# Kernel tuning notes

Measured on AMD Instinct MI355X. Metric: run time of the kernel, lower is better.

## Reference

```python
import jax
import jax.numpy as jnp
from jax import lax
import numpy as np

N_COLORS = 256  # n_possible_colors; classifier emits N_COLORS+1 logits (last = 'new color')
LRELU_SLOPE = 0.01  # torch nn.LeakyReLU default negative_slope


def setup_inputs() -> dict:
    key = jax.random.key(0)
    ks = jax.random.split(key, 8)
    N, E = 8192, 512
    deg = 32
    s1 = 1.0 / np.sqrt(2 * E)
    s2 = 1.0 / np.sqrt(E)
    s3 = 1.0 / np.sqrt(400)
    return {
        "embeddings": jax.random.normal(ks[0], (N, E), jnp.float32),
        "neighbors": jax.random.randint(ks[1], (N, deg), 0, N, jnp.int32),
        "W1": jax.random.normal(ks[2], (2 * E, E), jnp.float32) * s1,
        "b1": jnp.zeros((E,), jnp.float32),
        "W2": jax.random.normal(ks[3], (E, 400), jnp.float32) * s2,
        "b2": jnp.zeros((400,), jnp.float32),
        "W3": jax.random.normal(ks[4], (400, N_COLORS + 1), jnp.float32) * s3,
        "b3": jnp.zeros((N_COLORS + 1,), jnp.float32),
        "baseline": jnp.ones((), jnp.float32),
    }


def _leaky(x):
    return jnp.where(x >= 0, x, LRELU_SLOPE * x)


def reference(embeddings, neighbors, W1, b1, W2, b2, W3, b3, baseline):
    N, E = embeddings.shape
    C = N_COLORS + 1  # 257 output classes
    graph_emb = embeddings.mean(axis=0)  # torch.mean(embeddings, dim=0), constant across steps
    idx = jnp.arange(C)
    colors0 = jnp.full((N,), -1, jnp.int32).at[0].set(0)  # _assign_color(0, vertex_order[0])
    key0 = jax.random.key(42)

    def step(carry, v):
        colors, n_used, logp, key = carry
        key, sk = jax.random.split(key)
        # classifier MLP: cat(node_emb, graph_emb) -> 512 -> 400 -> 257
        x = jnp.concatenate([embeddings[v], graph_emb])  # [2E]
        h = _leaky(x @ W1 + b1)
        h = _leaky(h @ W2 + b2)
        logits = h @ W3 + b3  # [257]
        # _mask_irrelevant_colors: disable unused colors in [n_used, 256)
        irrel = (idx >= n_used) & (idx < N_COLORS)
        # _mask_colors: disable colors of already-colored neighbors (-1 = uncolored -> padded out)
        nb_c = colors[neighbors[v]]  # [deg]
        adj_mask = jnp.zeros((C + 1,), bool).at[jnp.where(nb_c < 0, C, nb_c)].set(True)[:C]
        logits = jnp.where(irrel | adj_mask, -jnp.inf, logits)
        probs = jax.nn.softmax(logits)  # classifier output
        raw = jax.random.categorical(sk, logits)  # np.random.choice(p=probs)
        chosen = jnp.where(raw == N_COLORS, n_used, raw).astype(jnp.int32)
        n_used = jnp.where(raw == N_COLORS, n_used + 1, n_used)
        colors = colors.at[v].set(chosen)
        p = probs[raw]
        logp = logp + jnp.log(p + 1e-8) - jnp.log(jnp.asarray(1e-8, p.dtype))
        return (colors, n_used, logp, key), None

    init = (colors0, jnp.int32(1), jnp.float32(0.0), key0)
    (colors, n_used, logp, _), _ = lax.scan(step, init, jnp.arange(1, N))
    loss = (n_used.astype(jnp.float32) - baseline) * logp / N
    return colors, loss
```

## Files before the change

### kernel.cpp

```cpp
#include <hip/hip_runtime.h>
#include <stdint.h>
#include <math.h>

#define NV 8192
#define EMB 512
#define CLS 257
#define DEG 32
#define TV 8
#define RSTRIDE 260

struct KP { uint32_t a, b; };

__host__ __device__ constexpr KP tfc(uint32_t k0, uint32_t k1,
                                     uint32_t x0, uint32_t x1) {
  const uint32_t ks2 = k0 ^ k1 ^ 0x1BD11BDAu;
  uint32_t v0 = x0 + k0, v1 = x1 + k1;
#define QR(r) { v0 += v1; v1 = (v1 << (r)) | (v1 >> (32 - (r))); v1 ^= v0; }
  QR(13) QR(15) QR(26) QR(6)
  v0 += k1;  v1 += ks2 + 1u;
  QR(17) QR(29) QR(16) QR(24)
  v0 += ks2; v1 += k0 + 2u;
  QR(13) QR(15) QR(26) QR(6)
  v0 += k0;  v1 += k1 + 3u;
  QR(17) QR(29) QR(16) QR(24)
  v0 += k1;  v1 += ks2 + 4u;
  QR(13) QR(15) QR(26) QR(6)
  v0 += ks2; v1 += k0 + 5u;
#undef QR
  return KP{v0, v1};
}

struct Seg { KP e[256]; };
constexpr Seg mkseg(KP s) {
  Seg g{};
  g.e[0] = s;
  for (int i = 1; i < 256; ++i) g.e[i] = tfc(g.e[i - 1].a, g.e[i - 1].b, 0u, 0u);
  return g;
}
#define NXTSEG(prev) mkseg(tfc(prev.e[255].a, prev.e[255].b, 0u, 0u))
constexpr Seg SG0 = mkseg(KP{0u, 42u});
constexpr Seg SG1 = NXTSEG(SG0);   constexpr Seg SG2 = NXTSEG(SG1);
constexpr Seg SG3 = NXTSEG(SG2);   constexpr Seg SG4 = NXTSEG(SG3);
constexpr Seg SG5 = NXTSEG(SG4);   constexpr Seg SG6 = NXTSEG(SG5);
constexpr Seg SG7 = NXTSEG(SG6);   constexpr Seg SG8 = NXTSEG(SG7);
constexpr Seg SG9 = NXTSEG(SG8);   constexpr Seg SG10 = NXTSEG(SG9);
constexpr Seg SG11 = NXTSEG(SG10); constexpr Seg SG12 = NXTSEG(SG11);
constexpr Seg SG13 = NXTSEG(SG12); constexpr Seg SG14 = NXTSEG(SG13);
constexpr Seg SG15 = NXTSEG(SG14); constexpr Seg SG16 = NXTSEG(SG15);
constexpr Seg SG17 = NXTSEG(SG16); constexpr Seg SG18 = NXTSEG(SG17);
constexpr Seg SG19 = NXTSEG(SG18); constexpr Seg SG20 = NXTSEG(SG19);
constexpr Seg SG21 = NXTSEG(SG20); constexpr Seg SG22 = NXTSEG(SG21);
constexpr Seg SG23 = NXTSEG(SG22); constexpr Seg SG24 = NXTSEG(SG23);
constexpr Seg SG25 = NXTSEG(SG24); constexpr Seg SG26 = NXTSEG(SG25);
constexpr Seg SG27 = NXTSEG(SG26); constexpr Seg SG28 = NXTSEG(SG27);
constexpr Seg SG29 = NXTSEG(SG28); constexpr Seg SG30 = NXTSEG(SG29);
constexpr Seg SG31 = NXTSEG(SG30);

struct KT { uint32_t hi[8192]; uint32_t lo[8192]; };
constexpr KT mkkt() {
  KT t{};
  const Seg* sg[32] = {
    &SG0,  &SG1,  &SG2,  &SG3,  &SG4,  &SG5,  &SG6,  &SG7,
    &SG8,  &SG9,  &SG10, &SG11, &SG12, &SG13, &SG14, &SG15,
    &SG16, &SG17, &SG18, &SG19, &SG20, &SG21, &SG22, &SG23,
    &SG24, &SG25, &SG26, &SG27, &SG28, &SG29, &SG30, &SG31 };
  for (int s = 0; s < 32; ++s)
    for (int i = 0; i < 256; ++i) {
      const int v = 1 + s * 256 + i;
      if (v < 8192) { t.hi[v] = sg[s]->e[i].a; t.lo[v] = sg[s]->e[i].b; }
    }
  return t;
}
__device__ const KT KEYS = mkkt();

__global__ __launch_bounds__(256) void colmean_part(const float* __restrict__ emb,
                                                    float* __restrict__ part) {
  const int b = blockIdx.x;
  const int t = threadIdx.x;
  for (int j = t; j < EMB; j += 256) {
    float s = 0.f;
    const int r0 = b * 128;
    for (int r = 0; r < 128; ++r) s += emb[(size_t)(r0 + r) * EMB + j];
    part[(size_t)b * EMB + j] = s;
  }
}

__global__ __launch_bounds__(256) void colmean_fin(const float* __restrict__ part,
                                                   float* __restrict__ g) {
  const int t = threadIdx.x;
  for (int j = t; j < EMB; j += 256) {
    float s = 0.f;
    for (int b = 0; b < 64; ++b) s += part[(size_t)b * EMB + j];
    g[j] = s / 8192.0f;
  }
}

__global__ __launch_bounds__(256) void mlp3i(
    const float* __restrict__ emb, const float* __restrict__ g,
    const float* __restrict__ W1, const float* __restrict__ b1,
    const float* __restrict__ W2, const float* __restrict__ b2,
    const float* __restrict__ W3, const float* __restrict__ b3,
    float* __restrict__ pl, float* __restrict__ er)
{
  __shared__ float xs[TV][68];
  __shared__ float gs[EMB];
  __shared__ float h1s[TV][EMB];
  __shared__ float h2s[TV][400];
  __shared__ float redw[TV][4];
  __shared__ float li256s[TV];
  __shared__ float mrs[TV];

  const int t  = threadIdx.x;
  const int v0 = blockIdx.x * TV;
  const int j2 = 2 * t;

  for (int j = t; j < EMB; j += 256) gs[j] = g[j];

  float accA[TV], accB[TV];
#pragma unroll
  for (int vv = 0; vv < TV; ++vv) { accA[vv] = 0.f; accB[vv] = 0.f; }

  for (int kc = 0; kc < 8; ++kc) {
    __syncthreads();
    if (t < 128) {
      const int vv = t >> 4;
      const int kk = (t & 15) << 2;
      const float4 s4 = *reinterpret_cast<const float4*>(
          &emb[(size_t)(v0 + vv) * EMB + kc * 64 + kk]);
      xs[vv][kk] = s4.x; xs[vv][kk + 1] = s4.y;
      xs[vv][kk + 2] = s4.z; xs[vv][kk + 3] = s4.w;
    }
    __syncthreads();
    float cA[TV], cB[TV];
#pragma unroll
    for (int vv = 0; vv < TV; ++vv) { cA[vv] = 0.f; cB[vv] = 0.f; }
    for (int q = 0; q < 16; ++q) {
      const int k = kc * 64 + q * 4;
      float2 w[4];
#pragma unroll
      for (int u = 0; u < 4; ++u)
        w[u] = *reinterpret_cast<const float2*>(&W1[(size_t)(k + u) * EMB + j2]);
      float4 xv[TV];
#pragma unroll
      for (int vv = 0; vv < TV; ++vv)
        xv[vv] = *reinterpret_cast<const float4*>(&xs[vv][q * 4]);
#pragma unroll
      for (int u = 0; u < 4; ++u) {
#pragma unroll
        for (int vv = 0; vv < TV; ++vv) {
          const float x = (u == 0) ? xv[vv].x : (u == 1) ? xv[vv].y
                         : (u == 2) ? xv[vv].z : xv[vv].w;
          cA[vv] = fmaf(x, w[u].x, cA[vv]);
          cB[vv] = fmaf(x, w[u].y, cB[vv]);
        }
      }
    }
#pragma unroll
    for (int vv = 0; vv < TV; ++vv) { accA[vv] += cA[vv]; accB[vv] += cB[vv]; }
  }

  float gA = 0.f, gB = 0.f;
  for (int kc = 0; kc < 8; ++kc) {
    float cgA = 0.f, cgB = 0.f;
    for (int q = 0; q < 16; ++q) {
      const int k = kc * 64 + q * 4;
      const float4 gv = *reinterpret_cast<const float4*>(&gs[k]);
      float2 w[4];
#pragma unroll
      for (int u = 0; u < 4; ++u)
        w[u] = *reinterpret_cast<const float2*>(
            &W1[(size_t)(EMB + k + u) * EMB + j2]);
      cgA = fmaf(gv.x, w[0].x, cgA); cgB = fmaf(gv.x, w[0].y, cgB);
      cgA = fmaf(gv.y, w[1].x, cgA); cgB = fmaf(gv.y, w[1].y, cgB);
      cgA = fmaf(gv.z, w[2].x, cgA); cgB = fmaf(gv.z, w[2].y, cgB);
      cgA = fmaf(gv.w, w[3].x, cgA); cgB = fmaf(gv.w, w[3].y, cgB);
    }
    gA += cgA; gB += cgB;
  }

  {
    const float bA = b1[j2], bB = b1[j2 + 1];
#pragma unroll
    for (int vv = 0; vv < TV; ++vv) {
      float hA = (accA[vv] + gA) + bA;
      float hB = (accB[vv] + gB) + bB;
      hA = (hA >= 0.f) ? hA : 0.01f * hA;
      hB = (hB >= 0.f) ? hB : 0.01f * hB;
      *reinterpret_cast<float2*>(&h1s[vv][j2]) = float2{hA, hB};
    }
  }
  __syncthreads();

  if (t < 200) {
    float a2A[TV], a2B[TV];
#pragma unroll
    for (int vv = 0; vv < TV; ++vv) { a2A[vv] = 0.f; a2B[vv] = 0.f; }
    for (int kc = 0; kc < 8; ++kc) {
      float cA[TV], cB[TV];
#pragma unroll
      for (int vv = 0; vv < TV; ++vv) { cA[vv] = 0.f; cB[vv] = 0.f; }
      for (int q = 0; q < 16; ++q) {
        const int k = kc * 64 + q * 4;
        float2 w[4];
#pragma unroll
        for (int u = 0; u < 4; ++u)
          w[u] = *reinterpret_cast<const float2*>(&W2[(size_t)(k + u) * 400 + j2]);
        float4 hv[TV];
#pragma unroll
        for (int vv = 0; vv < TV; ++vv)
          hv[vv] = *reinterpret_cast<const float4*>(&h1s[vv][k]);
#pragma unroll
        for (int u = 0; u < 4; ++u) {
#pragma unroll
          for (int vv = 0; vv < TV; ++vv) {
            const float x = (u == 0) ? hv[vv].x : (u == 1) ? hv[vv].y
                           : (u == 2) ? hv[vv].z : hv[vv].w;
            cA[vv] = fmaf(x, w[u].x, cA[vv]);
            cB[vv] = fmaf(x, w[u].y, cB[vv]);
          }
        }
      }
#pragma unroll
      for (int vv = 0; vv < TV; ++vv) { a2A[vv] += cA[vv]; a2B[vv] += cB[vv]; }
    }
    const float bA = b2[j2], bB = b2[j2 + 1];
#pragma unroll
    for (int vv = 0; vv < TV; ++vv) {
      float hA = a2A[vv] + bA;
      float hB = a2B[vv] + bB;
      hA = (hA >= 0.f) ? hA : 0.01f * hA;
      hB = (hB >= 0.f) ? hB : 0.01f * hB;
      *reinterpret_cast<float2*>(&h2s[vv][j2]) = float2{hA, hB};
    }
  }
  __syncthreads();

  float a3[TV], a3x[TV];
#pragma unroll
  for (int vv = 0; vv < TV; ++vv) { a3[vv] = 0.f; a3x[vv] = 0.f; }
  for (int kc = 0; kc < 8; ++kc) {
    float c3[TV], c3x[TV];
#pragma unroll
    for (int vv = 0; vv < TV; ++vv) { c3[vv] = 0.f; c3x[vv] = 0.f; }
    for (int kk = 0; kk < 50; ++kk) {
      const int k = kc * 50 + kk;
      const float w0 = W3[(size_t)k * CLS + t];
      const float wx = (t == 0) ? W3[(size_t)k * CLS + 256] : 0.f;
#pragma unroll
      for (int vv = 0; vv < TV; ++vv) {
        const float hv = h2s[vv][k];
        c3[vv]  = fmaf(hv, w0, c3[vv]);
        c3x[vv] = fmaf(hv, wx, c3x[vv]);
      }
    }
#pragma unroll
    for (int vv = 0; vv < TV; ++vv) { a3[vv] += c3[vv]; a3x[vv] += c3x[vv]; }
  }

  const float bj = b3[t];
  float li_[TV];
#pragma unroll
  for (int vv = 0; vv < TV; ++vv) li_[vv] = a3[vv] + bj;

#pragma unroll
  for (int vv = 0; vv < TV; ++vv) {
    float m = li_[vv];
#pragma unroll
    for (int off = 1; off < 64; off <<= 1) m = fmaxf(m, __shfl_xor(m, off));
    if ((t & 63) == 0) redw[vv][t >> 6] = m;
  }
  if (t == 0) {
    const float bx = b3[256];
#pragma unroll
    for (int vv = 0; vv < TV; ++vv) li256s[vv] = a3x[vv] + bx;
  }
  __syncthreads();
  if (t < TV) {
    const float m = fmaxf(fmaxf(redw[t][0], redw[t][1]),
                          fmaxf(redw[t][2], redw[t][3]));
    mrs[t] = fmaxf(m, li256s[t]);
  }
  __syncthreads();

#pragma unroll
  for (int vv = 0; vv < TV; ++vv) {
    const int v = v0 + vv;
    const float li = li_[vv];
    const KP sk = tfc(KEYS.hi[v], KEYS.lo[v], 0u, 1u);
    const KP o  = tfc(sk.a, sk.b, 0u, (uint32_t)t);
    const uint32_t bb = o.a ^ o.b;
    const float f = __uint_as_float(0x3f800000u | (bb >> 9)) - 1.0f;
    const float u = fmaxf(1.17549435e-38f, f);
    const float gg = -logf(-logf(u));
    pl[(size_t)v * RSTRIDE + t] = li + gg;
    er[(size_t)v * RSTRIDE + t] = expf(li - mrs[vv]);
  }
  if (t == 0) {
    const float bx = b3[256];
#pragma unroll
    for (int vv = 0; vv < TV; ++vv) {
      const int v = v0 + vv;
      const float li = a3x[vv] + bx;
      const KP sk = tfc(KEYS.hi[v], KEYS.lo[v], 0u, 1u);
      const KP o  = tfc(sk.a, sk.b, 0u, 256u);
      const uint32_t bb = o.a ^ o.b;
      const float f = __uint_as_float(0x3f800000u | (bb >> 9)) - 1.0f;
      const float u = fmaxf(1.17549435e-38f, f);
      const float gg = -logf(-logf(u));
      pl[(size_t)v * RSTRIDE + 256] = li + gg;
      er[(size_t)v * RSTRIDE + 256] = expf(li - mrs[vv]);
    }
  }
}

#define DPPF(CTRL, OLDI, X) \
  __builtin_amdgcn_update_dpp((int)(OLDI), (X), (CTRL), 0xF, 0xF, false)
#define SRED(CTRL) { S += __int_as_float(DPPF(CTRL, 0, __float_as_int(S))); }

__device__ __forceinline__ uint32_t ordmap(float f) {
  const uint32_t s = __float_as_uint(f);
  return s ^ (0x80000000u | (uint32_t)((int32_t)s >> 31));
}

#define WG_SCOPE __HIP_MEMORY_SCOPE_WORKGROUP

__global__ __launch_bounds__(256) void sortrows(float* __restrict__ plbuf) {
  __shared__ uint64_t keys[4][512];
  const int t = threadIdx.x;
  const int w = t >> 6;
  const int lane = t & 63;
  const int v = blockIdx.x * 4 + w;
  const float* row = plbuf + (size_t)v * RSTRIDE;

#pragma unroll
  for (int j = 0; j < 8; ++j) {
    const int i = lane + 64 * j;
    uint32_t om = 0u;
    if (i < CLS) om = ordmap(row[i]);
    keys[w][i] = ((uint64_t)om << 9) | (uint64_t)(511 - i);
  }
  __syncthreads();

  for (int k = 2; k <= 512; k <<= 1) {
    for (int j = k >> 1; j > 0; j >>= 1) {
#pragma unroll
      for (int m = 0; m < 4; ++m) {
        const int p  = lane + 64 * m;
        const int i  = ((p & ~(j - 1)) << 1) | (p & (j - 1));
        const int ix = i | j;
        const uint64_t a = keys[w][i], b = keys[w][ix];
        const bool sw = ((i & k) == 0) ? (a < b) : (a > b);
        if (sw) { keys[w][i] = b; keys[w][ix] = a; }
      }
      __syncthreads();
    }
  }

  uint16_t* o16 = reinterpret_cast<uint16_t*>(plbuf) + (size_t)v * (RSTRIDE * 2);
#pragma unroll
  for (int j = 0; j < 5; ++j) {
    const int i = lane + 64 * j;
    if (i < 320) o16[i] = (uint16_t)(511u - (uint32_t)(keys[w][i] & 511u));
  }
}

__global__ __launch_bounds__(128) void scan9(
    const int* __restrict__ nbrG, const uint32_t* __restrict__ scG,
    unsigned* __restrict__ rawnu, float* __restrict__ out)
{
  __shared__ int colors[NV];
  __shared__ uint32_t scR[32][160];
  __shared__ int nbrRing[1024];
  __shared__ unsigned bbuf[2][16];
  __shared__ int prod_done, cons_done;

  const int t = threadIdx.x;
  const int lane = t & 63;
  const int ln32 = lane & 31;
  const uint16_t* scR16 = reinterpret_cast<const uint16_t*>(&scR[0][0]);

  for (int i = t; i < NV; i += 128) colors[i] = -1;
  if (t == 0) { colors[0] = 0; prod_done = 0; cons_done = 0; }
  __syncthreads();

  if (t >= 64) {
    for (int pc = 0; pc < 1024; ++pc) {
      while (__hip_atomic_load(&cons_done, __ATOMIC_ACQUIRE, WG_SCOPE) < pc - 3)
        __builtin_amdgcn_s_sleep(1);
      uint32_t x[8], y[8], z[8];
#pragma unroll
      for (int r = 0; r < 8; ++r) {
        const size_t base = (size_t)(pc * 8 + r) * RSTRIDE;
        x[r] = scG[base + lane];
        y[r] = scG[base + 64 + lane];
        z[r] = (lane < 32) ? scG[base + 128 + lane] : 0u;
      }
      const int4 nb4 = *reinterpret_cast<const int4*>(nbrG + pc * 256 + 4 * lane);
#pragma unroll
      for (int r = 0; r < 8; ++r) {
        const int slot = (pc * 8 + r) & 31;
        scR[slot][lane] = x[r];
        scR[slot][64 + lane] = y[r];
        if (lane < 32) scR[slot][128 + lane] = z[r];
      }
      *reinterpret_cast<int4*>(&nbrRing[((pc & 3) << 8) + 4 * lane]) = nb4;
      if (lane == 0)
        __hip_atomic_store(&prod_done, pc + 1, __ATOMIC_RELEASE, WG_SCOPE);
    }
    return;
  }

  while (__hip_atomic_load(&prod_done, __ATOMIC_ACQUIRE, WG_SCOPE) < 2) {}

  int cp1 = 0;
  int n_used = 1;

  int c0, c1, d0, d1;
  bool sb0, sb1, hf;
  int nbrA, nbrB, cgv1;
  {
    bbuf[1][lane & 15] = 0u;
    const int nb1 = nbrRing[(1 << 5) + ln32];
    const int cg = colors[nb1];
    if (cg >= 0) atomicOr(&bbuf[1][cg >> 5], 1u << (cg & 31));
    const uint32_t cw = scR[1][lane];
    c0 = (int)(cw & 0xFFFFu); c1 = (int)(cw >> 16);
    const unsigned w0 = bbuf[1][c0 >> 5];
    const unsigned w1 = bbuf[1][c1 >> 5];
    sb0 = (!((w0 >> (c0 & 31)) & 1u)) && (c0 < 1 || c0 == 256);
    sb1 = (!((w1 >> (c1 & 31)) & 1u)) && (c1 < 1 || c1 == 256);
    hf = false;
    const uint32_t dw = scR[2][lane];
    d0 = (int)(dw & 0xFFFFu); d1 = (int)(dw >> 16);
    nbrA = nbrRing[(2 << 5) + ln32];
    cgv1 = colors[nbrA];
    nbrB = nbrRing[(3 << 5) + ln32];
  }

  for (int v = 1; v < NV; ++v) {
    const int slotN = (v + 1) & 1;

    bbuf[slotN][lane & 15] = 0u;
    if (cgv1 >= 0) atomicOr(&bbuf[slotN][cgv1 >> 5], 1u << (cgv1 & 31));
    const unsigned wd0 = bbuf[slotN][d0 >> 5];
    const unsigned wd1 = bbuf[slotN][d1 >> 5];

    const int nu0 = n_used;
    const int fixc = cp1;
    int raw = 256;
    {
      const bool okE = sb0 && !(hf && c0 == fixc);
      const bool okO = sb1 && !(hf && c1 == fixc);
      uint64_t b_ = __ballot(okE || okO);
      if (b_) {
        const int sel = okE ? c0 : c1;
        raw = __builtin_amdgcn_readlane(sel, (int)__builtin_ctzll(b_));
      } else {
        const int sBv = (v & 31) * 320;
        const int x2 = scR16[sBv + 128 + lane];
        const int x3 = scR16[sBv + 192 + lane];
        const int x4 = scR16[sBv + 256 + lane];
        const unsigned q2 = bbuf[v & 1][x2 >> 5];
        const unsigned q3 = bbuf[v & 1][x3 >> 5];
        const unsigned q4 = bbuf[v & 1][x4 >> 5];
        const bool o2 = (!((q2 >> (x2 & 31)) & 1u)) &&
                        (x2 < nu0 || x2 == 256) && !(hf && x2 == fixc);
        const bool o3 = (!((q3 >> (x3 & 31)) & 1u)) &&
                        (x3 < nu0 || x3 == 256) && !(hf && x3 == fixc);
        const bool o4 = (!((q4 >> (x4 & 31)) & 1u)) &&
                        (x4 < nu0 || x4 == 256) && !(hf && x4 == fixc);
        if ((b_ = __ballot(o2)))
          raw = __builtin_amdgcn_readlane(x2, (int)__builtin_ctzll(b_));
        else if ((b_ = __ballot(o3)))
          raw = __builtin_amdgcn_readlane(x3, (int)__builtin_ctzll(b_));
        else if ((b_ = __ballot(o4)))
          raw = __builtin_amdgcn_readlane(x4, (int)__builtin_ctzll(b_));
      }
    }
    const bool isnew = (raw == 256);
    const int chosen = isnew ? nu0 : raw;
    if (lane == 0) {
      colors[v] = chosen;
      rawnu[v] = (unsigned)raw | ((unsigned)nu0 << 16);
    }
    if (isnew) ++n_used;
    cp1 = chosen;

    const int nuN = n_used;
    const bool sbn0 = (!((wd0 >> (d0 & 31)) & 1u)) && (d0 < nuN || d0 == 256);
    const bool sbn1 = (!((wd1 >> (d1 & 31)) & 1u)) && (d1 < nuN || d1 == 256);
    const bool hfn = (__ballot(nbrA == v) != 0ULL);

    const int cgv2 = colors[nbrB];

    const int vp2 = (v + 2 < NV) ? v + 2 : NV - 1;
    const int vp3 = (v + 3 < NV) ? v + 3 : NV - 1;
    const uint32_t ew = scR[vp2 & 31][lane];
    const int nbrC = nbrRing[(((vp3 >> 3) & 3) << 8) + ((vp3 & 7) << 5) + ln32];

    c0 = d0; c1 = d1; sb0 = sbn0; sb1 = sbn1; hf = hfn;
    d0 = (int)(ew & 0xFFFFu); d1 = (int)(ew >> 16);
    cgv1 = cgv2; nbrA = nbrB; nbrB = nbrC;

    if ((v & 7) == 7) {
      if (lane == 0)
        __hip_atomic_store(&cons_done, (v + 1) >> 3, __ATOMIC_RELEASE, WG_SCOPE);
      int tgt = ((v + 1) >> 3) + 2;
      tgt = tgt > 1024 ? 1024 : tgt;
      while (__hip_atomic_load(&prod_done, __ATOMIC_ACQUIRE, WG_SCOPE) < tgt) {}
    }
  }

  for (int i = lane; i < NV; i += 64) out[i] = (float)colors[i];
}

__global__ __launch_bounds__(256) void logp_part(
    const float* __restrict__ outF, const int* __restrict__ nbrG,
    const float* __restrict__ er, const unsigned* __restrict__ rawnu,
    double* __restrict__ partd)
{
  __shared__ unsigned bb[4][16];
  const int t = threadIdx.x;
  const int w = t >> 6;
  const int lane = t & 63;
  const int ln32 = lane & 31;
  const int b = blockIdx.x;

  double a = 0.0;
  for (int i = 0; i < 32; ++i) {
    const int v = b * 128 + w * 32 + i;
    if (v == 0) continue;
    const unsigned val = rawnu[v];
    const int raw = (int)(val & 0xFFFFu);
    const int nu  = (int)(val >> 16);

    bb[w][lane & 15] = 0u;
    const int u = nbrG[(size_t)v * DEG + ln32];
    const int cu = (u < v) ? (int)outF[u] : -1;
    if (cu >= 0) atomicOr(&bb[w][cu >> 5], 1u << (cu & 31));
    unsigned bwp[4];
#pragma unroll
    for (int j = 0; j < 4; ++j) bwp[j] = bb[w][(lane >> 5) + 2 * j];
    const unsigned bw8 = bb[w][8];

    const size_t base = (size_t)v * RSTRIDE;
    bool mk[4];
    float e[4];
#pragma unroll
    for (int j = 0; j < 4; ++j) {
      const int c = lane + 64 * j;
      mk[j] = (((bwp[j] >> ln32) & 1u) != 0u) || (c >= nu);
      e[j] = mk[j] ? 0.f : er[base + c];
    }
    const bool mkX = ((bw8 & 1u) != 0u);
    const float eX = er[base + 256];
    const float e4 = (!mkX && lane == 0) ? eX : 0.f;

    float S = ((e[0] + e[1]) + (e[2] + e[3])) + e4;
    SRED(0x111) SRED(0x112) SRED(0x114) SRED(0x118) SRED(0x142) SRED(0x143)
    const float Sall = __int_as_float(
        __builtin_amdgcn_readlane(__float_as_int(S), 63));

    const bool isnew = (raw == 256);
    const int jsel  = isnew ? 4 : (raw >> 6);
    const int owner = isnew ? 0 : (raw & 63);
    const float cand = (jsel == 0) ? e[0] : (jsel == 1) ? e[1]
                     : (jsel == 2) ? e[2] : (jsel == 3) ? e[3] : e4;
    const float praw = __int_as_float(
        __builtin_amdgcn_readlane(__float_as_int(cand), owner));

    const float p = praw / Sall;
    a += (double)(logf(p + 1e-8f) - logf(1e-8f));
  }
  if (lane == 0) partd[b * 4 + w] = a;
}

__global__ __launch_bounds__(64) void finalize(
    const double* __restrict__ partd, const unsigned* __restrict__ rawnu,
    const float* __restrict__ baseline, float* __restrict__ out)
{
  if (threadIdx.x == 0) {
    double lp = 0.0;
    for (int i = 0; i < 256; ++i) lp += partd[i];
    const unsigned val = rawnu[NV - 1];
    const unsigned nf = (val >> 16) + (((val & 0xFFFFu) == 256u) ? 1u : 0u);
    out[NV] = ((float)nf - baseline[0]) * (float)lp / 8192.0f;
  }
}

extern "C" void kernel_launch(void* const* d_in, const int* in_sizes, int n_in,
                              void* d_out, int out_size, void* d_ws, size_t ws_size,
                              hipStream_t stream) {
  const float* emb      = (const float*)d_in[0];
  const int*   nbr      = (const int*)d_in[1];
  const float* W1       = (const float*)d_in[2];
  const float* b1       = (const float*)d_in[3];
  const float* W2       = (const float*)d_in[4];
  const float* b2       = (const float*)d_in[5];
  const float* W3       = (const float*)d_in[6];
  const float* b3       = (const float*)d_in[7];
  const float* baseline = (const float*)d_in[8];
  float* out = (float*)d_out;

  char* ws = (char*)d_ws;
  float* g     = (float*)ws;
  float* plbuf = (float*)(ws + 2048);
  float* erbuf = (float*)(ws + 2048 + NV * RSTRIDE * 4);
  float* part  = erbuf;
  unsigned* rawnu = (unsigned*)(ws + 2048);
  double*   partd = (double*)(ws + 2048 + 65536);

  colmean_part<<<64, 256, 0, stream>>>(emb, part);
  colmean_fin<<<1, 256, 0, stream>>>(part, g);
  mlp3i<<<NV / TV, 256, 0, stream>>>(emb, g, W1, b1, W2, b2, W3, b3, plbuf, erbuf);
  sortrows<<<NV / 4, 256, 0, stream>>>(plbuf);
  scan9<<<1, 128, 0, stream>>>(nbr, (const uint32_t*)plbuf, rawnu, out);
  logp_part<<<64, 256, 0, stream>>>((const float*)out, nbr, erbuf, rawnu, partd);
  finalize<<<1, 64, 0, stream>>>(partd, rawnu, baseline, out);
}
```

Before: 2.907 ms.

## Split serial coloring scan across two alternating consumer wavefronts with LDS relay

The single consumer wavefront in the sequential coloring scan becomes two wavefronts that take even and odd vertices in turn. They pass the step state (vertex, n_used, last chosen color) through a packed LDS word written with an atomic release. While one wave makes its decision, the other prepares the neighbor-color bitmask and candidate list for its next vertex, taking that per-step setup off the serial critical path. The cost is a cross-wave spin handoff on every step, plus a producer that now has to track two consumer progress counters.

After: 2.515 ms (median of 2 runs). -13.5%, faster.

```diff
diff --git a/kernel.cpp b/kernel.cpp
--- a/kernel.cpp
+++ b/kernel.cpp
@@ -364,29 +364,38 @@
   }
 }
 
-__global__ __launch_bounds__(128) void scan9(
+__global__ __launch_bounds__(192) void scan10(
     const int* __restrict__ nbrG, const uint32_t* __restrict__ scG,
     unsigned* __restrict__ rawnu, float* __restrict__ out)
 {
   __shared__ int colors[NV];
   __shared__ uint32_t scR[32][160];
   __shared__ int nbrRing[1024];
-  __shared__ unsigned bbuf[2][16];
-  __shared__ int prod_done, cons_done;
+  __shared__ unsigned bbufW[2][2][16];
+  __shared__ int prod_done, consA_done, consB_done;
+  __shared__ unsigned relay;
 
   const int t = threadIdx.x;
+  const int wid = t >> 6;
   const int lane = t & 63;
   const int ln32 = lane & 31;
   const uint16_t* scR16 = reinterpret_cast<const uint16_t*>(&scR[0][0]);
 
-  for (int i = t; i < NV; i += 128) colors[i] = -1;
-  if (t == 0) { colors[0] = 0; prod_done = 0; cons_done = 0; }
+  for (int i = t; i < NV; i += 192) colors[i] = -1;
+  if (t == 0) {
+    colors[0] = 0; prod_done = 0; consA_done = 0; consB_done = 0;
+    relay = (0u << 19) | (1u << 9) | 0u;
+  }
   __syncthreads();
 
-  if (t >= 64) {
+  if (wid == 2) {
     for (int pc = 0; pc < 1024; ++pc) {
-      while (__hip_atomic_load(&cons_done, __ATOMIC_ACQUIRE, WG_SCOPE) < pc - 3)
+      for (;;) {
+        const int ca = __hip_atomic_load(&consA_done, __ATOMIC_ACQUIRE, WG_SCOPE);
+        const int cb = __hip_atomic_load(&consB_done, __ATOMIC_ACQUIRE, WG_SCOPE);
+        if ((ca < cb ? ca : cb) >= pc - 3) break;
         __builtin_amdgcn_s_sleep(1);
+      }
       uint32_t x[8], y[8], z[8];
 #pragma unroll
       for (int r = 0; r < 8; ++r) {
@@ -410,65 +419,68 @@
     return;
   }
 
-  while (__hip_atomic_load(&prod_done, __ATOMIC_ACQUIRE, WG_SCOPE) < 2) {}
-
-  int cp1 = 0;
-  int n_used = 1;
-
-  int c0, c1, d0, d1;
-  bool sb0, sb1, hf;
-  int nbrA, nbrB, cgv1;
-  {
-    bbuf[1][lane & 15] = 0u;
-    const int nb1 = nbrRing[(1 << 5) + ln32];
-    const int cg = colors[nb1];
-    if (cg >= 0) atomicOr(&bbuf[1][cg >> 5], 1u << (cg & 31));
-    const uint32_t cw = scR[1][lane];
-    c0 = (int)(cw & 0xFFFFu); c1 = (int)(cw >> 16);
-    const unsigned w0 = bbuf[1][c0 >> 5];
-    const unsigned w1 = bbuf[1][c1 >> 5];
-    sb0 = (!((w0 >> (c0 & 31)) & 1u)) && (c0 < 1 || c0 == 256);
-    sb1 = (!((w1 >> (c1 & 31)) & 1u)) && (c1 < 1 || c1 == 256);
-    hf = false;
-    const uint32_t dw = scR[2][lane];
-    d0 = (int)(dw & 0xFFFFu); d1 = (int)(dw >> 16);
-    nbrA = nbrRing[(2 << 5) + ln32];
-    cgv1 = colors[nbrA];
-    nbrB = nbrRing[(3 << 5) + ln32];
-  }
-
-  for (int v = 1; v < NV; ++v) {
-    const int slotN = (v + 1) & 1;
-
-    bbuf[slotN][lane & 15] = 0u;
-    if (cgv1 >= 0) atomicOr(&bbuf[slotN][cgv1 >> 5], 1u << (cgv1 & 31));
-    const unsigned wd0 = bbuf[slotN][d0 >> 5];
-    const unsigned wd1 = bbuf[slotN][d1 >> 5];
-
-    const int nu0 = n_used;
-    const int fixc = cp1;
+  const int v0 = 1 + wid;
+  unsigned* const slot0 = bbufW[wid][0];
+  unsigned* const slot1 = bbufW[wid][1];
+
+  int pdc = 0;
+  while (pdc < 1)
+    pdc = __hip_atomic_load(&prod_done, __ATOMIC_ACQUIRE, WG_SCOPE);
+
+  int c0 = 0, c1 = 0;
+  bool fb0 = false, fb1 = false, hf = false;
+
+#define PREP10(V) {                                                            \
+    const int v_ = (V);                                                        \
+    while (pdc <= (v_ >> 3))                                                   \
+      pdc = __hip_atomic_load(&prod_done, __ATOMIC_ACQUIRE, WG_SCOPE);         \
+    const uint32_t cw_ = scR[v_ & 31][lane];                                   \
+    const int nb_ = nbrRing[(((v_ >> 3) & 3) << 8) + ((v_ & 7) << 5) + ln32];  \
+    unsigned* const sl_ = ((v_ >> 1) & 1) ? slot1 : slot0;                     \
+    sl_[lane & 15] = 0u;                                                       \
+    const int cg_ = colors[nb_];                                               \
+    hf = (__ballot(nb_ == v_ - 1) != 0ULL);                                    \
+    if (cg_ >= 0) atomicOr(&sl_[cg_ >> 5], 1u << (cg_ & 31));                  \
+    c0 = (int)(cw_ & 0xFFFFu); c1 = (int)(cw_ >> 16);                          \
+    const unsigned w0_ = sl_[c0 >> 5];                                         \
+    const unsigned w1_ = sl_[c1 >> 5];                                         \
+    fb0 = !((w0_ >> (c0 & 31)) & 1u);                                          \
+    fb1 = !((w1_ >> (c1 & 31)) & 1u);                                          \
+  }
+
+  PREP10(v0)
+
+  for (int v = v0; v < NV; v += 2) {
+    unsigned r;
+    do {
+      r = __hip_atomic_load(&relay, __ATOMIC_ACQUIRE, WG_SCOPE);
+    } while ((r >> 19) != (unsigned)(v - 1));
+    const int nu = (int)((r >> 9) & 0x3FFu);
+    const int cp = (int)(r & 0x1FFu);
+
     int raw = 256;
     {
-      const bool okE = sb0 && !(hf && c0 == fixc);
-      const bool okO = sb1 && !(hf && c1 == fixc);
-      uint64_t b_ = __ballot(okE || okO);
+      const bool ok0 = fb0 && (c0 < nu || c0 == 256) && !(hf && c0 == cp);
+      const bool ok1 = fb1 && (c1 < nu || c1 == 256) && !(hf && c1 == cp);
+      uint64_t b_ = __ballot(ok0 || ok1);
       if (b_) {
-        const int sel = okE ? c0 : c1;
+        const int sel = ok0 ? c0 : c1;
         raw = __builtin_amdgcn_readlane(sel, (int)__builtin_ctzll(b_));
       } else {
         const int sBv = (v & 31) * 320;
+        unsigned* const sl_ = ((v >> 1) & 1) ? slot1 : slot0;
         const int x2 = scR16[sBv + 128 + lane];
         const int x3 = scR16[sBv + 192 + lane];
         const int x4 = scR16[sBv + 256 + lane];
-        const unsigned q2 = bbuf[v & 1][x2 >> 5];
-        const unsigned q3 = bbuf[v & 1][x3 >> 5];
-        const unsigned q4 = bbuf[v & 1][x4 >> 5];
+        const unsigned q2 = sl_[x2 >> 5];
+        const unsigned q3 = sl_[x3 >> 5];
+        const unsigned q4 = sl_[x4 >> 5];
         const bool o2 = (!((q2 >> (x2 & 31)) & 1u)) &&
-                        (x2 < nu0 || x2 == 256) && !(hf && x2 == fixc);
+                        (x2 < nu || x2 == 256) && !(hf && x2 == cp);
         const bool o3 = (!((q3 >> (x3 & 31)) & 1u)) &&
-                        (x3 < nu0 || x3 == 256) && !(hf && x3 == fixc);
+                        (x3 < nu || x3 == 256) && !(hf && x3 == cp);
         const bool o4 = (!((q4 >> (x4 & 31)) & 1u)) &&
-                        (x4 < nu0 || x4 == 256) && !(hf && x4 == fixc);
+                        (x4 < nu || x4 == 256) && !(hf && x4 == cp);
         if ((b_ = __ballot(o2)))
           raw = __builtin_amdgcn_readlane(x2, (int)__builtin_ctzll(b_));
         else if ((b_ = __ballot(o3)))
@@ -478,40 +490,38 @@
       }
     }
     const bool isnew = (raw == 256);
-    const int chosen = isnew ? nu0 : raw;
+    const int chosen = isnew ? nu : raw;
+    const unsigned nuN = (unsigned)nu + (isnew ? 1u : 0u);
     if (lane == 0) {
       colors[v] = chosen;
-      rawnu[v] = (unsigned)raw | ((unsigned)nu0 << 16);
-    }
-    if (isnew) ++n_used;
-    cp1 = chosen;
-
-    const int nuN = n_used;
-    const bool sbn0 = (!((wd0 >> (d0 & 31)) & 1u)) && (d0 < nuN || d0 == 256);
-    const bool sbn1 = (!((wd1 >> (d1 & 31)) & 1u)) && (d1 < nuN || d1 == 256);
-    const bool hfn = (__ballot(nbrA == v) != 0ULL);
-
-    const int cgv2 = colors[nbrB];
-
-    const int vp2 = (v + 2 < NV) ? v + 2 : NV - 1;
-    const int vp3 = (v + 3 < NV) ? v + 3 : NV - 1;
-    const uint32_t ew = scR[vp2 & 31][lane];
-    const int nbrC = nbrRing[(((vp3 >> 3) & 3) << 8) + ((vp3 & 7) << 5) + ln32];
-
-    c0 = d0; c1 = d1; sb0 = sbn0; sb1 = sbn1; hf = hfn;
-    d0 = (int)(ew & 0xFFFFu); d1 = (int)(ew >> 16);
-    cgv1 = cgv2; nbrA = nbrB; nbrB = nbrC;
-
-    if ((v & 7) == 7) {
-      if (lane == 0)
-        __hip_atomic_store(&cons_done, (v + 1) >> 3, __ATOMIC_RELEASE, WG_SCOPE);
-      int tgt = ((v + 1) >> 3) + 2;
-      tgt = tgt > 1024 ? 1024 : tgt;
-      while (__hip_atomic_load(&prod_done, __ATOMIC_ACQUIRE, WG_SCOPE) < tgt) {}
-    }
-  }
-
-  for (int i = lane; i < NV; i += 64) out[i] = (float)colors[i];
+      rawnu[v] = (unsigned)raw | ((unsigned)nu << 16);
+      __hip_atomic_store(&relay,
+          ((unsigned)v << 19) | (nuN << 9) | (unsigned)chosen,
+          __ATOMIC_RELEASE, WG_SCOPE);
+    }
+
+    if ((v & 7) == 7 - wid) {
+      const int dn = (v + 1 + wid) >> 3;
+      if (lane == 0) {
+        if (wid == 0)
+          __hip_atomic_store(&consA_done, dn, __ATOMIC_RELEASE, WG_SCOPE);
+        else
+          __hip_atomic_store(&consB_done, dn, __ATOMIC_RELEASE, WG_SCOPE);
+      }
+    }
+
+    if (v + 2 < NV) PREP10(v + 2)
+  }
+
+  if (lane == 0) {
+    if (wid == 0)
+      __hip_atomic_store(&consA_done, 1024, __ATOMIC_RELEASE, WG_SCOPE);
+    else
+      __hip_atomic_store(&consB_done, 1024, __ATOMIC_RELEASE, WG_SCOPE);
+  }
+
+  if (wid == 0)
+    for (int i = lane; i < NV; i += 64) out[i] = (float)colors[i];
 }
 
 __global__ __launch_bounds__(256) void logp_part(
@@ -614,7 +624,7 @@
   colmean_fin<<<1, 256, 0, stream>>>(part, g);
   mlp3i<<<NV / TV, 256, 0, stream>>>(emb, g, W1, b1, W2, b2, W3, b3, plbuf, erbuf);
   sortrows<<<NV / 4, 256, 0, stream>>>(plbuf);
-  scan9<<<1, 128, 0, stream>>>(nbr, (const uint32_t*)plbuf, rawnu, out);
+  scan10<<<1, 192, 0, stream>>>(nbr, (const uint32_t*)plbuf, rawnu, out);
   logp_part<<<64, 256, 0, stream>>>((const float*)out, nbr, erbuf, rawnu, partd);
   finalize<<<1, 64, 0, stream>>>(partd, rawnu, baseline, out);
 }
```
